# Performance work log

Measured on AMD Instinct MI355X. Metric: run time of the kernel, lower is better.

Reference implementation:

```python
import jax, jax.numpy as jnp
import numpy as np
from jax import lax

B, C, H, W = 8, 128, 256, 256
OUT_CH = 64
IN_CH = C * 9  # 1152: module's in_channels = 9 * image channels (unfold with 3x3 kernel)


def setup_inputs() -> dict:
    key = jax.random.key(0)
    k1, k2, k3 = jax.random.split(key, 3)
    x = jax.random.normal(k1, (B, C, H, W), dtype=jnp.float32)
    style = jax.random.normal(k2, (B, IN_CH), dtype=jnp.float32)
    # learned parameter: torch.randn(out_channels, in_channels, 1, 1) -> store as (out, in)
    weight = jax.random.normal(k3, (OUT_CH, IN_CH), dtype=jnp.float32)
    return {"x": x, "style": style, "weight": weight}


def reference(x, style, weight):
    b, c, h, w = x.shape
    out_ch, in_ch = weight.shape  # in_ch == c * 9
    # unfold column ordering is (c, kh, kw), so the flattened weight is exactly a
    # 3x3 conv kernel: (out, c*9) -> (out, c, 3, 3)
    w33 = weight.reshape(out_ch, c, 3, 3)
    # style.view(B,1,in_ch,1,1) * weight -> per-sample modulated 3x3 kernels
    w_mod = style.reshape(b, 1, c, 3, 3) * w33[None]  # (B, out, c, 3, 3)

    def conv_one(xi, wi):
        # xi: (c, h, w), wi: (out, c, 3, 3); SAME padding matches padding=(1,1)
        return lax.conv_general_dilated(
            xi[None], wi, window_strides=(1, 1), padding="SAME",
            dimension_numbers=("NCHW", "OIHW", "NCHW"))[0]

    out = jax.vmap(conv_one)(x, w_mod)  # (B, out, h, w)
    return out
```

## Files before the change

kernel.cpp:

```cpp
#include <hip/hip_runtime.h>
#include <hip/hip_bf16.h>

#define BATCH 8
#define CIN   128
#define HH    256
#define WW    256
#define OUTC  64
#define INCH  1152
#define HW    (HH*WW)
#define WMOD_BYTES ((size_t)BATCH * 9 * OUTC * CIN * 2)

typedef __attribute__((ext_vector_type(8))) short short8;
typedef __attribute__((ext_vector_type(4))) float f32x4;

__device__ __forceinline__ unsigned short bf16r(float f) {
    unsigned u = __builtin_bit_cast(unsigned, f);
    u += 0x7fffu + ((u >> 16) & 1u);
    return (unsigned short)(u >> 16);
}

__global__ void __launch_bounds__(256) wmod_kernel(const float* __restrict__ weight,
                                                   const float* __restrict__ style,
                                                   unsigned short* __restrict__ wmod) {
    int i = blockIdx.x * 256 + threadIdx.x;
    if (i >= BATCH * 9 * OUTC * CIN) return;
    int c    = i & (CIN - 1);
    int rest = i >> 7;
    int o    = rest & (OUTC - 1);
    int bt   = rest >> 6;
    int tap  = bt % 9;
    int b    = bt / 9;
    int k    = c * 9 + tap;
    wmod[i] = bf16r(weight[o * INCH + k] * style[b * INCH + k]);
}

template <bool GW>
__global__ void __launch_bounds__(256, 2) conv9_kernel(
    const float* __restrict__ x,
    const unsigned short* __restrict__ wmod,
    const float* __restrict__ weight,
    const float* __restrict__ style,
    float* __restrict__ out)
{
    __shared__ __align__(16) unsigned short xs_sm[2][204 * 32];

    const int tid = threadIdx.x;
    const int bx  = blockIdx.x;
    const int b   = blockIdx.y;
    const int h0  = (bx >> 3) * 4;
    const int w0  = (bx & 7) * 32;

    const int wv  = tid >> 6;
    const int wr  = wv >> 1;
    const int wc  = wv & 1;
    const int l15 = tid & 15;
    const int kg  = (tid >> 4) & 3;

    const bool tv = tid < 240;
    const int tt  = tv ? tid : 0;
    const int cg  = tt / 60;
    const int rem = tt % 60;
    const int sr  = rem / 10;
    const int qw  = rem % 10;
    const int sh  = h0 - 1 + sr;
    const bool hok = tv && ((unsigned)sh < HH);
    const int wl  = w0 - 4 + qw * 4;
    const int wlc = min(max(wl, 0), WW - 4);
    const int colbase = wl - (w0 - 1);
    const float* xbase = x + ((size_t)(b * CIN + cg * 8)) * HW +
                         (hok ? sh : 0) * WW + wlc;

    f32x4  f[8];
    short8 A[9][2];

    auto loadG = [&](int chunk) {
        if (hok) {
#pragma unroll
            for (int j = 0; j < 8; ++j)
                f[j] = *(const f32x4*)(xbase + (size_t)(chunk * 32 + j) * HW);
        }
    };

    auto writeG = [&](unsigned short* buf) {
        if (tv) {
#pragma unroll
            for (int u = 0; u < 4; ++u) {
                int col = colbase + u;
                if (col >= 0 && col < 34) {
                    bool wok = hok && ((unsigned)(wl + u) < WW);
                    short8 sv;
#pragma unroll
                    for (int j = 0; j < 8; ++j)
                        sv[j] = wok ? (short)bf16r(f[j][u]) : (short)0;
                    int s = sr * 34 + col;
                    *(short8*)&buf[s * 32 + cg * 8] = sv;
                }
            }
        }
    };

    auto loadA = [&](int chunk) {
        if (GW) {
            const unsigned short* wb =
                wmod + ((size_t)(b * 9) * OUTC) * CIN + chunk * 32 + kg * 8;
#pragma unroll
            for (int tap = 0; tap < 9; ++tap)
#pragma unroll
                for (int mi = 0; mi < 2; ++mi)
                    A[tap][mi] = *(const short8*)(
                        wb + ((size_t)tap * OUTC + wr * 32 + mi * 16 + l15) * CIN);
        } else {
#pragma unroll
            for (int tap = 0; tap < 9; ++tap)
#pragma unroll
                for (int mi = 0; mi < 2; ++mi) {
                    int o = wr * 32 + mi * 16 + l15;
#pragma unroll
                    for (int j = 0; j < 8; ++j) {
                        int c = chunk * 32 + kg * 8 + j;
                        int k = c * 9 + tap;
                        A[tap][mi][j] = (short)bf16r(weight[o * INCH + k] *
                                                     style[b * INCH + k]);
                    }
                }
        }
    };

    f32x4 acc[2][4];
#pragma unroll
    for (int mi = 0; mi < 2; ++mi)
#pragma unroll
        for (int ni = 0; ni < 4; ++ni) acc[mi][ni] = (f32x4){0.f, 0.f, 0.f, 0.f};

    auto compute = [&](const unsigned short* buf) {
#pragma unroll
        for (int kh = 0; kh < 3; ++kh)
#pragma unroll
            for (int kw = 0; kw < 3; ++kw) {
                const int tap = kh * 3 + kw;
                short8 Bv[4];
#pragma unroll
                for (int ni = 0; ni < 4; ++ni) {
                    int s = (ni + kh) * 34 + wc * 16 + l15 + kw;
                    Bv[ni] = *(const short8*)&buf[s * 32 + kg * 8];
                }
#pragma unroll
                for (int mi = 0; mi < 2; ++mi)
#pragma unroll
                    for (int ni = 0; ni < 4; ++ni)
                        acc[mi][ni] = __builtin_amdgcn_mfma_f32_16x16x32_bf16(
                            A[tap][mi], Bv[ni], acc[mi][ni], 0, 0, 0);
            }
    };

    loadG(0);
    loadA(0);
    __builtin_amdgcn_sched_barrier(0);
    writeG(xs_sm[0]);
    __syncthreads();

    loadG(1);
    __builtin_amdgcn_sched_barrier(0);
    compute(xs_sm[0]);
    __builtin_amdgcn_sched_barrier(0);
    loadA(1);
    writeG(xs_sm[1]);
    __syncthreads();

    loadG(2);
    __builtin_amdgcn_sched_barrier(0);
    compute(xs_sm[1]);
    __builtin_amdgcn_sched_barrier(0);
    loadA(2);
    writeG(xs_sm[0]);
    __syncthreads();

    loadG(3);
    __builtin_amdgcn_sched_barrier(0);
    compute(xs_sm[0]);
    __builtin_amdgcn_sched_barrier(0);
    loadA(3);
    writeG(xs_sm[1]);
    __syncthreads();

    compute(xs_sm[1]);

    float* op = out + ((size_t)b * OUTC) * HW + (size_t)h0 * WW + w0 + wc * 16 + l15;
#pragma unroll
    for (int mi = 0; mi < 2; ++mi)
#pragma unroll
        for (int ni = 0; ni < 4; ++ni)
#pragma unroll
            for (int rr = 0; rr < 4; ++rr) {
                int o = wr * 32 + mi * 16 + kg * 4 + rr;
                op[(size_t)o * HW + ni * WW] = acc[mi][ni][rr];
            }
}

extern "C" void kernel_launch(void* const* d_in, const int* in_sizes, int n_in,
                              void* d_out, int out_size, void* d_ws, size_t ws_size,
                              hipStream_t stream) {
    const float* x      = (const float*)d_in[0];
    const float* style  = (const float*)d_in[1];
    const float* weight = (const float*)d_in[2];
    float* out = (float*)d_out;

    const int wmod_total = BATCH * 9 * OUTC * CIN;

    if (ws_size >= WMOD_BYTES) {
        unsigned short* wmodp = (unsigned short*)d_ws;
        wmod_kernel<<<(wmod_total + 255) / 256, 256, 0, stream>>>(weight, style, wmodp);
        conv9_kernel<true><<<dim3(512, BATCH), 256, 0, stream>>>(
            x, wmodp, nullptr, nullptr, out);
    } else {
        conv9_kernel<false><<<dim3(512, BATCH), 256, 0, stream>>>(
            x, nullptr, weight, style, out);
    }
}
```

Baseline: 228.3 us.

## Switch conv to 32x32x16 MFMA with 8-row tiles and 16-channel K chunks

Each block now covers an 8x32 output tile instead of 4x32, with every wave handling two output rows against all 64 output channels. The inner product uses 32x32x16 bf16 MFMA instructions in place of 16x16x32. The input channels are staged in 16-channel chunks over an 8-step double-buffered loop, with a padded LDS stride of 20, and the plain __syncthreads is replaced by an lgkmcnt wait plus s_barrier. The aim is more reuse of the modulated weights per block, fewer blocks, and higher MFMA efficiency. The cost is twice as many barrier phases, and the new LDS layout may cause bank conflicts.

```diff
diff --git a/kernel.cpp b/kernel.cpp
--- a/kernel.cpp
+++ b/kernel.cpp
@@ -10,8 +10,9 @@
 #define HW    (HH*WW)
 #define WMOD_BYTES ((size_t)BATCH * 9 * OUTC * CIN * 2)
 
-typedef __attribute__((ext_vector_type(8))) short short8;
-typedef __attribute__((ext_vector_type(4))) float f32x4;
+typedef __attribute__((ext_vector_type(8)))  short short8;
+typedef __attribute__((ext_vector_type(4)))  float f32x4;
+typedef __attribute__((ext_vector_type(16))) float f32x16;
 
 __device__ __forceinline__ unsigned short bf16r(float f) {
     unsigned u = __builtin_bit_cast(unsigned, f);
@@ -34,32 +35,38 @@
     wmod[i] = bf16r(weight[o * INCH + k] * style[b * INCH + k]);
 }
 
+#define PBAR()                                              \
+    do {                                                    \
+        asm volatile("s_waitcnt lgkmcnt(0)" ::: "memory");  \
+        __builtin_amdgcn_sched_barrier(0);                  \
+        __builtin_amdgcn_s_barrier();                       \
+        __builtin_amdgcn_sched_barrier(0);                  \
+    } while (0)
+
 template <bool GW>
-__global__ void __launch_bounds__(256, 2) conv9_kernel(
+__global__ void __launch_bounds__(256, 2) conv10_kernel(
     const float* __restrict__ x,
     const unsigned short* __restrict__ wmod,
     const float* __restrict__ weight,
     const float* __restrict__ style,
     float* __restrict__ out)
 {
-    __shared__ __align__(16) unsigned short xs_sm[2][204 * 32];
+    __shared__ __align__(16) unsigned short xs_sm[2][340 * 20];
 
     const int tid = threadIdx.x;
     const int bx  = blockIdx.x;
     const int b   = blockIdx.y;
-    const int h0  = (bx >> 3) * 4;
+    const int h0  = (bx >> 3) * 8;
     const int w0  = (bx & 7) * 32;
 
     const int wv  = tid >> 6;
-    const int wr  = wv >> 1;
-    const int wc  = wv & 1;
-    const int l15 = tid & 15;
-    const int kg  = (tid >> 4) & 3;
-
-    const bool tv = tid < 240;
+    const int l31 = tid & 31;
+    const int kh2 = (tid >> 5) & 1;
+
+    const bool tv = tid < 200;
     const int tt  = tv ? tid : 0;
-    const int cg  = tt / 60;
-    const int rem = tt % 60;
+    const int cg  = tt / 100;
+    const int rem = tt % 100;
     const int sr  = rem / 10;
     const int qw  = rem % 10;
     const int sh  = h0 - 1 + sr;
@@ -77,7 +84,7 @@
         if (hok) {
 #pragma unroll
             for (int j = 0; j < 8; ++j)
-                f[j] = *(const f32x4*)(xbase + (size_t)(chunk * 32 + j) * HW);
+                f[j] = *(const f32x4*)(xbase + (size_t)(chunk * 16 + j) * HW);
         }
     };
 
@@ -93,7 +100,7 @@
                     for (int j = 0; j < 8; ++j)
                         sv[j] = wok ? (short)bf16r(f[j][u]) : (short)0;
                     int s = sr * 34 + col;
-                    *(short8*)&buf[s * 32 + cg * 8] = sv;
+                    *(short8*)&buf[s * 20 + cg * 8] = sv;
                 }
             }
         }
@@ -102,22 +109,22 @@
     auto loadA = [&](int chunk) {
         if (GW) {
             const unsigned short* wb =
-                wmod + ((size_t)(b * 9) * OUTC) * CIN + chunk * 32 + kg * 8;
+                wmod + ((size_t)(b * 9) * OUTC) * CIN + chunk * 16 + kh2 * 8;
 #pragma unroll
             for (int tap = 0; tap < 9; ++tap)
 #pragma unroll
                 for (int mi = 0; mi < 2; ++mi)
                     A[tap][mi] = *(const short8*)(
-                        wb + ((size_t)tap * OUTC + wr * 32 + mi * 16 + l15) * CIN);
+                        wb + ((size_t)tap * OUTC + mi * 32 + l31) * CIN);
         } else {
 #pragma unroll
             for (int tap = 0; tap < 9; ++tap)
 #pragma unroll
                 for (int mi = 0; mi < 2; ++mi) {
-                    int o = wr * 32 + mi * 16 + l15;
+                    int o = mi * 32 + l31;
 #pragma unroll
                     for (int j = 0; j < 8; ++j) {
-                        int c = chunk * 32 + kg * 8 + j;
+                        int c = chunk * 16 + kh2 * 8 + j;
                         int k = c * 9 + tap;
                         A[tap][mi][j] = (short)bf16r(weight[o * INCH + k] *
                                                      style[b * INCH + k]);
@@ -126,11 +133,13 @@
         }
     };
 
-    f32x4 acc[2][4];
+    f32x16 acc[2][2];
 #pragma unroll
     for (int mi = 0; mi < 2; ++mi)
 #pragma unroll
-        for (int ni = 0; ni < 4; ++ni) acc[mi][ni] = (f32x4){0.f, 0.f, 0.f, 0.f};
+        for (int ni = 0; ni < 2; ++ni)
+#pragma unroll
+            for (int r = 0; r < 16; ++r) acc[mi][ni][r] = 0.f;
 
     auto compute = [&](const unsigned short* buf) {
 #pragma unroll
@@ -138,17 +147,17 @@
 #pragma unroll
             for (int kw = 0; kw < 3; ++kw) {
                 const int tap = kh * 3 + kw;
-                short8 Bv[4];
-#pragma unroll
-                for (int ni = 0; ni < 4; ++ni) {
-                    int s = (ni + kh) * 34 + wc * 16 + l15 + kw;
-                    Bv[ni] = *(const short8*)&buf[s * 32 + kg * 8];
+                short8 Bv[2];
+#pragma unroll
+                for (int ni = 0; ni < 2; ++ni) {
+                    int s = (2 * wv + ni + kh) * 34 + l31 + kw;
+                    Bv[ni] = *(const short8*)&buf[s * 20 + kh2 * 8];
                 }
 #pragma unroll
                 for (int mi = 0; mi < 2; ++mi)
 #pragma unroll
-                    for (int ni = 0; ni < 4; ++ni)
-                        acc[mi][ni] = __builtin_amdgcn_mfma_f32_16x16x32_bf16(
+                    for (int ni = 0; ni < 2; ++ni)
+                        acc[mi][ni] = __builtin_amdgcn_mfma_f32_32x32x16_bf16(
                             A[tap][mi], Bv[ni], acc[mi][ni], 0, 0, 0);
             }
     };
@@ -157,44 +166,33 @@
     loadA(0);
     __builtin_amdgcn_sched_barrier(0);
     writeG(xs_sm[0]);
-    __syncthreads();
-
-    loadG(1);
-    __builtin_amdgcn_sched_barrier(0);
-    compute(xs_sm[0]);
-    __builtin_amdgcn_sched_barrier(0);
-    loadA(1);
-    writeG(xs_sm[1]);
-    __syncthreads();
-
-    loadG(2);
-    __builtin_amdgcn_sched_barrier(0);
-    compute(xs_sm[1]);
-    __builtin_amdgcn_sched_barrier(0);
-    loadA(2);
-    writeG(xs_sm[0]);
-    __syncthreads();
-
-    loadG(3);
-    __builtin_amdgcn_sched_barrier(0);
-    compute(xs_sm[0]);
-    __builtin_amdgcn_sched_barrier(0);
-    loadA(3);
-    writeG(xs_sm[1]);
-    __syncthreads();
-
-    compute(xs_sm[1]);
-
-    float* op = out + ((size_t)b * OUTC) * HW + (size_t)h0 * WW + w0 + wc * 16 + l15;
+    PBAR();
+
+#pragma unroll
+    for (int k = 0; k < 8; ++k) {
+        if (k < 7) loadG(k + 1);
+        __builtin_amdgcn_sched_barrier(0);
+        compute(xs_sm[k & 1]);
+        __builtin_amdgcn_sched_barrier(0);
+        if (k < 7) {
+            loadA(k + 1);
+            writeG(xs_sm[(k & 1) ^ 1]);
+            PBAR();
+        }
+    }
+
+    float* op = out + ((size_t)b * OUTC) * HW + w0 + l31;
 #pragma unroll
     for (int mi = 0; mi < 2; ++mi)
 #pragma unroll
-        for (int ni = 0; ni < 4; ++ni)
-#pragma unroll
-            for (int rr = 0; rr < 4; ++rr) {
-                int o = wr * 32 + mi * 16 + kg * 4 + rr;
-                op[(size_t)o * HW + ni * WW] = acc[mi][ni][rr];
+        for (int ni = 0; ni < 2; ++ni) {
+            int h = h0 + 2 * wv + ni;
+#pragma unroll
+            for (int r = 0; r < 16; ++r) {
+                int o = mi * 32 + (r & 3) + 8 * (r >> 2) + 4 * kh2;
+                op[(size_t)o * HW + h * WW] = acc[mi][ni][r];
             }
+        }
 }
 
 extern "C" void kernel_launch(void* const* d_in, const int* in_sizes, int n_in,
@@ -210,10 +208,10 @@
     if (ws_size >= WMOD_BYTES) {
         unsigned short* wmodp = (unsigned short*)d_ws;
         wmod_kernel<<<(wmod_total + 255) / 256, 256, 0, stream>>>(weight, style, wmodp);
-        conv9_kernel<true><<<dim3(512, BATCH), 256, 0, stream>>>(
+        conv10_kernel<true><<<dim3(256, BATCH), 256, 0, stream>>>(
             x, wmodp, nullptr, nullptr, out);
     } else {
-        conv9_kernel<false><<<dim3(512, BATCH), 256, 0, stream>>>(
+        conv10_kernel<false><<<dim3(256, BATCH), 256, 0, stream>>>(
             x, nullptr, weight, style, out);
     }
 }
```

Result: no change. 229.2 us (+0.4%).
